# Performance work log

Hardware: AMD Instinct MI355X
Metric: run time of the kernel (lower is better)

Reference implementation:

```python
import jax, jax.numpy as jnp
import numpy as np

EMB = 1024
NH = 16
HD = EMB // NH
FF = 4 * EMB
B, T = 2, 2048
LN_EPS = 1e-5


def setup_inputs() -> dict:
    key = jax.random.key(0)
    ks = jax.random.split(key, 16)
    s = 0.02
    return {
        "x": jax.random.normal(ks[0], (B, T, EMB), jnp.float32),
        "wq": jax.random.normal(ks[1], (EMB, EMB), jnp.float32) * s,
        "bq": jnp.zeros((EMB,), jnp.float32),
        "wk": jax.random.normal(ks[2], (EMB, EMB), jnp.float32) * s,
        "bk": jnp.zeros((EMB,), jnp.float32),
        "wv": jax.random.normal(ks[3], (EMB, EMB), jnp.float32) * s,
        "bv": jnp.zeros((EMB,), jnp.float32),
        "wo": jax.random.normal(ks[4], (EMB, EMB), jnp.float32) * s,
        "bo": jnp.zeros((EMB,), jnp.float32),
        "w1": jax.random.normal(ks[5], (EMB, FF), jnp.float32) * s,
        "b1": jnp.zeros((FF,), jnp.float32),
        "w2": jax.random.normal(ks[6], (FF, EMB), jnp.float32) * s,
        "b2": jnp.zeros((EMB,), jnp.float32),
        "ln1_g": jnp.ones((EMB,), jnp.float32),
        "ln1_b": jnp.zeros((EMB,), jnp.float32),
        "ln2_g": jnp.ones((EMB,), jnp.float32),
        "ln2_b": jnp.zeros((EMB,), jnp.float32),
        "alpha_attn": jnp.float32(0.5),
        "alpha_ff": jnp.float32(0.5),
    }


def _layernorm(x, g, b):
    mu = jnp.mean(x, axis=-1, keepdims=True)
    var = jnp.var(x, axis=-1, keepdims=True)
    return (x - mu) * jax.lax.rsqrt(var + LN_EPS) * g + b


def reference(x, wq, bq, wk, bk, wv, bv, wo, bo, w1, b1, w2, b2,
              ln1_g, ln1_b, ln2_g, ln2_b, alpha_attn, alpha_ff):
    residual = x
    x_ = _layernorm(x, ln1_g, ln1_b)
    # [B,T,E] -> [B,H,T,D]
    def heads(y):
        return y.reshape(B, T, NH, HD).transpose(0, 2, 1, 3)
    q = heads(x_ @ wq + bq)
    k = heads(x_ @ wk + bk)
    v = heads(x_ @ wv + bv)
    scores = jnp.einsum("bhqd,bhkd->bhqk", q, k) / np.sqrt(HD).astype(np.float32)
    causal = jnp.tril(jnp.ones((T, T), dtype=bool))
    scores = jnp.where(causal, scores, -jnp.inf)
    attn = jax.nn.softmax(scores, axis=-1)  # dropout is identity in eval mode
    out = jnp.einsum("bhqk,bhkd->bhqd", attn, v)
    out = out.transpose(0, 2, 1, 3).reshape(B, T, EMB)
    out = out @ wo + bo
    x = residual + alpha_attn * out
    x2 = _layernorm(x, ln2_g, ln2_b)
    ff = jax.nn.gelu(x2 @ w1 + b1, approximate=False) @ w2 + b2
    return x + alpha_ff * ff
```

## Files before the change

### kernel.cpp

```cpp
#include <hip/hip_runtime.h>
#include <cmath>

#define EMB 1024
#define NH 16
#define HD 64
#define FF_DIM 4096
#define BB 2
#define TT 2048
#define NTOK (BB * TT)
#define QKVS 3072
#define SC2F 0.18033688011112042f

typedef _Float16 f16x8 __attribute__((ext_vector_type(8)));
typedef _Float16 f16x4 __attribute__((ext_vector_type(4)));
typedef float f32x4 __attribute__((ext_vector_type(4)));

__device__ __forceinline__ float gelu_fast(float x) {
    float u = x * (1.f + 0.044715f * x * x);
    float e = exp2f(u * 2.302118751f);
    return x - x / (e + 1.f);
}

template <typename TIN>
__global__ __launch_bounds__(256) void ln_kernel(const TIN* __restrict__ xin,
                                                 _Float16* __restrict__ out,
                                                 const float* __restrict__ g,
                                                 const float* __restrict__ bv) {
    int tid = threadIdx.x;
    size_t base = (size_t)blockIdx.x * EMB;
    float v[4];
#pragma unroll
    for (int i = 0; i < 4; ++i) v[i] = (float)xin[base + i * 256 + tid];
    float s = v[0] + v[1] + v[2] + v[3];
    float ss = v[0] * v[0] + v[1] * v[1] + v[2] * v[2] + v[3] * v[3];
#pragma unroll
    for (int off = 32; off > 0; off >>= 1) {
        s += __shfl_down(s, off);
        ss += __shfl_down(ss, off);
    }
    __shared__ float red[8];
    int wave = tid >> 6;
    if ((tid & 63) == 0) { red[wave] = s; red[4 + wave] = ss; }
    __syncthreads();
    s = red[0] + red[1] + red[2] + red[3];
    ss = red[4] + red[5] + red[6] + red[7];
    float mu = s * (1.0f / EMB);
    float var = ss * (1.0f / EMB) - mu * mu;
    float rstd = rsqrtf(var + 1e-5f);
#pragma unroll
    for (int i = 0; i < 4; ++i) {
        int idx = i * 256 + tid;
        float y = (v[i] - mu) * rstd * g[idx] + bv[idx];
        out[base + idx] = (_Float16)y;
    }
}

__global__ __launch_bounds__(256) void prep0_kernel(const float* __restrict__ x,
                                                    _Float16* __restrict__ xn,
                                                    const float* __restrict__ ln1_g,
                                                    const float* __restrict__ ln1_b,
                                                    const float* __restrict__ wq,
                                                    const float* __restrict__ wk,
                                                    const float* __restrict__ wv,
                                                    const float* __restrict__ wo,
                                                    const float* __restrict__ bq,
                                                    const float* __restrict__ bk,
                                                    const float* __restrict__ bv,
                                                    _Float16* __restrict__ wqkvT,
                                                    _Float16* __restrict__ woT,
                                                    float* __restrict__ qkvbias) {
    __shared__ float tile[32][33];
    int blk = blockIdx.x;
    int tid = threadIdx.x;
    if (blk >= 4108) {
        size_t base = (size_t)(blk - 4108) * EMB;
        float v[4];
#pragma unroll
        for (int i = 0; i < 4; ++i) v[i] = x[base + i * 256 + tid];
        float s = v[0] + v[1] + v[2] + v[3];
        float ss = v[0] * v[0] + v[1] * v[1] + v[2] * v[2] + v[3] * v[3];
#pragma unroll
        for (int off = 32; off > 0; off >>= 1) {
            s += __shfl_down(s, off);
            ss += __shfl_down(ss, off);
        }
        float* red = &tile[0][0];
        int wave = tid >> 6;
        if ((tid & 63) == 0) { red[wave] = s; red[4 + wave] = ss; }
        __syncthreads();
        s = red[0] + red[1] + red[2] + red[3];
        ss = red[4] + red[5] + red[6] + red[7];
        float mu = s * (1.0f / EMB);
        float var = ss * (1.0f / EMB) - mu * mu;
        float rstd = rsqrtf(var + 1e-5f);
#pragma unroll
        for (int i = 0; i < 4; ++i) {
            int idx = i * 256 + tid;
            xn[base + idx] = (_Float16)((v[i] - mu) * rstd * ln1_g[idx] + ln1_b[idx]);
        }
        return;
    }
    if (blk >= 4096) {
        int i = (blk - 4096) * 256 + tid;
        qkvbias[i] = i < 1024 ? bq[i] : (i < 2048 ? bk[i - 1024] : bv[i - 2048]);
        return;
    }
    const float* W;
    _Float16* Wt;
    int t = blk & 1023;
    int z = blk >> 10;
    if (z == 0) { W = wq; Wt = wqkvT; }
    else if (z == 1) { W = wk; Wt = wqkvT + 1024 * 1024; }
    else if (z == 2) { W = wv; Wt = wqkvT + 2 * 1024 * 1024; }
    else { W = wo; Wt = woT; }
    int bx = (t & 31) * 32, by = (t >> 5) * 32;
    int tx = tid & 31, ty = tid >> 5;
#pragma unroll
    for (int i = 0; i < 32; i += 8)
        tile[ty + i][tx] = W[(size_t)(by + ty + i) * EMB + bx + tx];
    __syncthreads();
#pragma unroll
    for (int i = 0; i < 32; i += 8)
        Wt[(size_t)(bx + ty + i) * EMB + by + tx] = (_Float16)tile[tx][ty + i];
}

__global__ __launch_bounds__(256) void prep2_kernel(const float* __restrict__ w1,
                                                    const float* __restrict__ w2,
                                                    _Float16* __restrict__ w1T,
                                                    _Float16* __restrict__ w2T) {
    int b = blockIdx.x;
    const float* W;
    _Float16* Wt;
    int K, N, t;
    if (b < 4096) { W = w1; Wt = w1T; K = 1024; N = 4096; t = b; }
    else { W = w2; Wt = w2T; K = 4096; N = 1024; t = b - 4096; }
    int ntx = N >> 5;
    int bx = (t % ntx) * 32, by = (t / ntx) * 32;
    __shared__ float tile[32][33];
    int tx = threadIdx.x & 31, ty = threadIdx.x >> 5;
#pragma unroll
    for (int i = 0; i < 32; i += 8)
        tile[ty + i][tx] = W[(size_t)(by + ty + i) * N + bx + tx];
    __syncthreads();
#pragma unroll
    for (int i = 0; i < 32; i += 8)
        Wt[(size_t)(bx + ty + i) * K + by + tx] = (_Float16)tile[tx][ty + i];
}

__global__ __launch_bounds__(256) void vT_kernel(const _Float16* __restrict__ qkv,
                                                 _Float16* __restrict__ VtG) {
    __shared__ _Float16 tile[64][72];
    int tid = threadIdx.x;
    int bh = blockIdx.y;
    int b = bh >> 4, h = bh & 15;
    int t0 = blockIdx.x * 64;
    const _Float16* src = qkv + (size_t)b * TT * QKVS + 2048 + h * HD;
    int r = tid >> 3;
    int c8 = (tid & 7) * 8;
#pragma unroll
    for (int p = 0; p < 2; ++p)
        *(f16x8*)(&tile[r + p * 32][c8]) =
            *(const f16x8*)(src + (size_t)(t0 + r + p * 32) * QKVS + c8);
    __syncthreads();
#pragma unroll
    for (int p = 0; p < 2; ++p) {
        int d = r + p * 32;
        f16x8 v;
#pragma unroll
        for (int j = 0; j < 8; ++j) v[j] = tile[c8 + j][d];
        *(f16x8*)(VtG + ((size_t)bh * HD + d) * TT + t0 + c8) = v;
    }
}

template <int MODE>
__global__ __launch_bounds__(256) void gemm_f16t(const _Float16* __restrict__ A,
                                                 const _Float16* __restrict__ Bt,
                                                 const float* __restrict__ bias,
                                                 void* __restrict__ outp,
                                                 void* __restrict__ vtg,
                                                 int M, int N, int K, int lda, int ldb) {
    __shared__ _Float16 As[128][64];
    __shared__ _Float16 Bs[128][64];
    int tid = threadIdx.x;
    int lane = tid & 63, w = tid >> 6;
    int quad = lane >> 4, l15 = lane & 15;
    int wm = (w >> 1) * 64, wn = (w & 1) * 64;
    int bM = blockIdx.y * 128, bN = blockIdx.x * 128;
    int lr = lane >> 3;
    int lcs = ((lane & 7) ^ lr) * 8;
    int sw = l15 & 7;
    f32x4 acc[4][4] = {};

    const _Float16* Abase = A + (size_t)(bM + w * 32 + lr) * lda + lcs;
    const _Float16* Bbase = Bt + (size_t)(bN + w * 32 + lr) * ldb + lcs;

    for (int kt = 0; kt < K; kt += 64) {
#pragma unroll
        for (int i = 0; i < 4; ++i) {
            __builtin_amdgcn_global_load_lds(
                (const __attribute__((address_space(1))) void*)(Abase + (size_t)(i * 8) * lda + kt),
                (__attribute__((address_space(3))) void*)(&As[w * 32 + i * 8][0]), 16, 0, 0);
            __builtin_amdgcn_global_load_lds(
                (const __attribute__((address_space(1))) void*)(Bbase + (size_t)(i * 8) * ldb + kt),
                (__attribute__((address_space(3))) void*)(&Bs[w * 32 + i * 8][0]), 16, 0, 0);
        }
        __syncthreads();
#pragma unroll
        for (int ks = 0; ks < 2; ++ks) {
            f16x8 af[4], bf[4];
#pragma unroll
            for (int i = 0; i < 4; ++i) {
                int sc = ((ks * 4 + quad) ^ sw) * 8;
                af[i] = *(const f16x8*)(&As[wm + i * 16 + l15][sc]);
                bf[i] = *(const f16x8*)(&Bs[wn + i * 16 + l15][sc]);
            }
#pragma unroll
            for (int i = 0; i < 4; ++i)
#pragma unroll
                for (int j = 0; j < 4; ++j)
                    acc[i][j] = __builtin_amdgcn_mfma_f32_16x16x32_f16(af[i], bf[j], acc[i][j], 0, 0, 0);
        }
        __syncthreads();
    }

    if (MODE == 6 && vtg != nullptr && bN >= 2048) {
        int bb = bM >> 11;
        int tbase = (bM & 2047) + wm;
#pragma unroll
        for (int i = 0; i < 4; ++i)
#pragma unroll
            for (int j = 0; j < 4; ++j) {
                int hd = bN - 2048 + wn + j * 16;
                int col = 2048 + hd + l15;
                _Float16* dst = (_Float16*)vtg +
                    (((size_t)(bb * 16 + (hd >> 6)) * 64) + (hd & 63) + l15) * TT +
                    tbase + i * 16 + quad * 4;
                f16x4 ov;
#pragma unroll
                for (int r = 0; r < 4; ++r) ov[r] = (_Float16)(acc[i][j][r] + bias[col]);
                *(f16x4*)dst = ov;
            }
        return;
    }

#pragma unroll
    for (int i = 0; i < 4; ++i)
#pragma unroll
        for (int j = 0; j < 4; ++j)
#pragma unroll
            for (int r = 0; r < 4; ++r) {
                int row = bM + wm + i * 16 + quad * 4 + r;
                int col = bN + wn + j * 16 + l15;
                size_t idx = (size_t)row * N + col;
                float vv = acc[i][j][r] + bias[col];
                if (MODE == 6) {
                    if (bN < 1024) vv *= SC2F;
                    ((_Float16*)outp)[idx] = (_Float16)vv;
                } else {
                    ((_Float16*)outp)[idx] = (_Float16)gelu_fast(vv);
                }
            }
}

#define STAGE_PAIR(OB, TN, I)                                                            \
    {                                                                                    \
        size_t ko = (size_t)(TN) * 64;                                                   \
        __builtin_amdgcn_global_load_lds(                                                \
            (const __attribute__((address_space(1))) void*)(Ab + (size_t)((I) * 8) * lda + ko), \
            (__attribute__((address_space(3))) void*)(&As[OB][w * 32 + (I) * 8][0]), 16, 0, 0); \
        __builtin_amdgcn_global_load_lds(                                                \
            (const __attribute__((address_space(1))) void*)(Bb + (size_t)((I) * 8) * ldb + ko), \
            (__attribute__((address_space(3))) void*)(&Bs[OB][w * 32 + (I) * 8][0]), 16, 0, 0); \
    }
#define RD_A(CB, I, KS) (*(const f16x8*)(&As[CB][wr * 128 + (I) * 16 + l15][(((KS)*4 + quad) ^ sw) * 8]))
#define RD_B(CB, J, KS) (*(const f16x8*)(&Bs[CB][wc * 64 + (J) * 16 + l15][(((KS)*4 + quad) ^ sw) * 8]))
#define MMQ(I0, J0)                                                                      \
    _Pragma("unroll") for (int ks = 0; ks < 2; ++ks) {                                   \
        _Pragma("unroll") for (int ii = 0; ii < 4; ++ii) {                               \
            _Pragma("unroll") for (int jj = 0; jj < 2; ++jj)                             \
                acc[(I0) + ii][(J0) + jj] = __builtin_amdgcn_mfma_f32_16x16x32_f16(      \
                    af[ii][ks], bf[(J0) + jj][ks], acc[(I0) + ii][(J0) + jj], 0, 0, 0);  \
        }                                                                                \
    }

template <int MODE>
__global__ __launch_bounds__(512, 2) void gemm256(const _Float16* __restrict__ A,
                                                  const _Float16* __restrict__ Bt,
                                                  const float* __restrict__ bias,
                                                  void* __restrict__ outp,
                                                  void* __restrict__ vtg,
                                                  int M, int N, int K, int lda, int ldb) {
    __shared__ _Float16 As[2][256][64];
    __shared__ _Float16 Bs[2][256][64];
    int tid = threadIdx.x;
    int lane = tid & 63, w = tid >> 6;
    int quad = lane >> 4, l15 = lane & 15;
    int wr = w >> 2, wc = w & 3;
    int gx = gridDim.x;
    int nwg = gx * gridDim.y;
    int bid = blockIdx.y * gx + blockIdx.x;
    int cpx = nwg >> 3;
    int sbid = (bid & 7) * cpx + (bid >> 3);
    int bN = (sbid % gx) * 256;
    int bM = (sbid / gx) * 256;
    int lr = lane >> 3;
    int lcs = ((lane & 7) ^ lr) * 8;
    int sw = l15 & 7;
    f32x4 acc[8][4] = {};
    f16x8 af[4][2], bf[4][2];

    const _Float16* Ab = A + (size_t)(bM + w * 32 + lr) * lda + lcs;
    const _Float16* Bb = Bt + (size_t)(bN + w * 32 + lr) * ldb + lcs;
    const int NT = K >> 6;

#pragma unroll
    for (int i = 0; i < 4; ++i) STAGE_PAIR(0, 0, i);
    asm volatile("s_waitcnt vmcnt(0)" ::: "memory");
    __builtin_amdgcn_s_barrier();

    int cur = 0;
    for (int t = 0; t < NT; ++t) {
        int nxt = cur ^ 1;
        int tn = (t + 1 < NT) ? t + 1 : 0;
#pragma unroll
        for (int i = 0; i < 4; ++i) STAGE_PAIR(nxt, tn, i);
#pragma unroll
        for (int i = 0; i < 4; ++i) {
            af[i][0] = RD_A(cur, i, 0);
            af[i][1] = RD_A(cur, i, 1);
        }
        bf[0][0] = RD_B(cur, 0, 0); bf[0][1] = RD_B(cur, 0, 1);
        bf[1][0] = RD_B(cur, 1, 0); bf[1][1] = RD_B(cur, 1, 1);
        MMQ(0, 0);
        bf[2][0] = RD_B(cur, 2, 0); bf[2][1] = RD_B(cur, 2, 1);
        bf[3][0] = RD_B(cur, 3, 0); bf[3][1] = RD_B(cur, 3, 1);
        MMQ(0, 2);
#pragma unroll
        for (int i = 0; i < 4; ++i) {
            af[i][0] = RD_A(cur, 4 + i, 0);
            af[i][1] = RD_A(cur, 4 + i, 1);
        }
        MMQ(4, 0);
        MMQ(4, 2);
        asm volatile("s_waitcnt vmcnt(0)" ::: "memory");
        __builtin_amdgcn_s_barrier();
        cur = nxt;
    }

    if (MODE == 1 && vtg != nullptr && bN >= 2048) {
        int bb = bM >> 11;
#pragma unroll
        for (int i = 0; i < 8; ++i)
#pragma unroll
            for (int j = 0; j < 4; ++j) {
                int hd = bN - 2048 + wc * 64 + j * 16;
                int col = 2048 + hd + l15;
                int tb = (bM & 2047) + wr * 128 + i * 16 + quad * 4;
                _Float16* dst = (_Float16*)vtg +
                    (((size_t)(bb * 16 + (hd >> 6)) * 64) + (hd & 63) + l15) * TT + tb;
                f16x4 ov;
#pragma unroll
                for (int r = 0; r < 4; ++r) ov[r] = (_Float16)(acc[i][j][r] + bias[col]);
                *(f16x4*)dst = ov;
            }
        return;
    }

#pragma unroll
    for (int i = 0; i < 8; ++i)
#pragma unroll
        for (int j = 0; j < 4; ++j)
#pragma unroll
            for (int r = 0; r < 4; ++r) {
                int row = bM + wr * 128 + i * 16 + quad * 4 + r;
                int col = bN + wc * 64 + j * 16 + l15;
                size_t idx = (size_t)row * N + col;
                float vv = acc[i][j][r] + bias[col];
                if (MODE == 1) {
                    if (bN < 1024) vv *= SC2F;
                    ((_Float16*)outp)[idx] = (_Float16)vv;
                } else {
                    ((_Float16*)outp)[idx] = (_Float16)gelu_fast(vv);
                }
            }
}

__global__ __launch_bounds__(512) void gemm_ff2(const _Float16* __restrict__ A,
                                                const _Float16* __restrict__ Bt,
                                                _Float16* __restrict__ p0,
                                                _Float16* __restrict__ p1,
                                                int M, int N, int K, int lda, int ldb) {
    __shared__ _Float16 As[2][256][64];
    __shared__ _Float16 Bs[2][128][64];
    int tid = threadIdx.x;
    int lane = tid & 63, w = tid >> 6;
    int quad = lane >> 4, l15 = lane & 15;
    int wr = w >> 1, wc = w & 1;
    int gx = gridDim.x;
    int nwg = gx * gridDim.y;
    int bid = blockIdx.y * gx + blockIdx.x;
    int cpx = nwg >> 3;
    int sbid = (bid & 7) * cpx + (bid >> 3);
    int bN = (sbid % gx) * 128;
    int bM = (sbid / gx) * 256;
    int kz = blockIdx.z * K;
    int lr = lane >> 3;
    int lcs = ((lane & 7) ^ lr) * 8;
    int sw = l15 & 7;
    f32x4 acc[4][4] = {};
    f16x8 af[4][2], bf[4][2];

    const _Float16* Ab = A + (size_t)(bM + w * 32 + lr) * lda + kz + lcs;
    const _Float16* Bb = Bt + (size_t)(bN + w * 16 + lr) * ldb + kz + lcs;
    const int NT = K >> 6;

#define FF2_STAGE(OB, TN)                                                                \
    {                                                                                    \
        size_t ko = (size_t)(TN) * 64;                                                   \
        _Pragma("unroll") for (int i = 0; i < 4; ++i)                                    \
            __builtin_amdgcn_global_load_lds(                                            \
                (const __attribute__((address_space(1))) void*)(Ab + (size_t)(i * 8) * lda + ko), \
                (__attribute__((address_space(3))) void*)(&As[OB][w * 32 + i * 8][0]), 16, 0, 0); \
        _Pragma("unroll") for (int i = 0; i < 2; ++i)                                    \
            __builtin_amdgcn_global_load_lds(                                            \
                (const __attribute__((address_space(1))) void*)(Bb + (size_t)(i * 8) * ldb + ko), \
                (__attribute__((address_space(3))) void*)(&Bs[OB][w * 16 + i * 8][0]), 16, 0, 0); \
    }

    FF2_STAGE(0, 0);
    asm volatile("s_waitcnt vmcnt(0)" ::: "memory");
    __builtin_amdgcn_s_barrier();

    int cur = 0;
    for (int t = 0; t < NT; ++t) {
        int nxt = cur ^ 1;
        int tn = (t + 1 < NT) ? t + 1 : 0;
        FF2_STAGE(nxt, tn);
#pragma unroll
        for (int i = 0; i < 4; ++i) {
#pragma unroll
            for (int ks = 0; ks < 2; ++ks)
                af[i][ks] = *(const f16x8*)(&As[cur][wr * 64 + i * 16 + l15][((ks * 4 + quad) ^ sw) * 8]);
        }
#pragma unroll
        for (int j = 0; j < 4; ++j) {
#pragma unroll
            for (int ks = 0; ks < 2; ++ks)
                bf[j][ks] = *(const f16x8*)(&Bs[cur][wc * 64 + j * 16 + l15][((ks * 4 + quad) ^ sw) * 8]);
        }
#pragma unroll
        for (int ks = 0; ks < 2; ++ks)
#pragma unroll
            for (int i = 0; i < 4; ++i)
#pragma unroll
                for (int j = 0; j < 4; ++j)
                    acc[i][j] = __builtin_amdgcn_mfma_f32_16x16x32_f16(af[i][ks], bf[j][ks], acc[i][j], 0, 0, 0);
        asm volatile("s_waitcnt vmcnt(0)" ::: "memory");
        __builtin_amdgcn_s_barrier();
        cur = nxt;
    }

    _Float16* pout = blockIdx.z ? p1 : p0;
#pragma unroll
    for (int i = 0; i < 4; ++i)
#pragma unroll
        for (int j = 0; j < 4; ++j)
#pragma unroll
            for (int r = 0; r < 4; ++r) {
                int row = bM + wr * 64 + i * 16 + quad * 4 + r;
                int col = bN + wc * 64 + j * 16 + l15;
                pout[(size_t)row * N + col] = (_Float16)acc[i][j][r];
            }
}

template <int MODE>
__global__ __launch_bounds__(256) void gemm64(const _Float16* __restrict__ A,
                                              const _Float16* __restrict__ Bt,
                                              const float* __restrict__ bias,
                                              void* __restrict__ outp,
                                              const void* __restrict__ residp,
                                              const float* __restrict__ alphap,
                                              int M, int N, int K, int lda, int ldb) {
    __shared__ _Float16 As[128][64];
    __shared__ _Float16 Bs[64][64];
    int tid = threadIdx.x;
    int lane = tid & 63, w = tid >> 6;
    int quad = lane >> 4, l15 = lane & 15;
    int wm = w * 32;
    int bM = blockIdx.y * 128, bN = blockIdx.x * 64;
    int lr = lane >> 3;
    int lcs = ((lane & 7) ^ lr) * 8;
    int sw = l15 & 7;
    f32x4 acc[2][4] = {};

    const _Float16* Abase = A + (size_t)(bM + w * 32 + lr) * lda + lcs;
    const _Float16* Bbase = Bt + (size_t)(bN + w * 16 + lr) * ldb + lcs;

    for (int kt = 0; kt < K; kt += 64) {
#pragma unroll
        for (int i = 0; i < 4; ++i)
            __builtin_amdgcn_global_load_lds(
                (const __attribute__((address_space(1))) void*)(Abase + (size_t)(i * 8) * lda + kt),
                (__attribute__((address_space(3))) void*)(&As[w * 32 + i * 8][0]), 16, 0, 0);
#pragma unroll
        for (int i = 0; i < 2; ++i)
            __builtin_amdgcn_global_load_lds(
                (const __attribute__((address_space(1))) void*)(Bbase + (size_t)(i * 8) * ldb + kt),
                (__attribute__((address_space(3))) void*)(&Bs[w * 16 + i * 8][0]), 16, 0, 0);
        __syncthreads();
#pragma unroll
        for (int ks = 0; ks < 2; ++ks) {
            int sc = ((ks * 4 + quad) ^ sw) * 8;
            f16x8 af[2], bf[4];
#pragma unroll
            for (int i = 0; i < 2; ++i)
                af[i] = *(const f16x8*)(&As[wm + i * 16 + l15][sc]);
#pragma unroll
            for (int j = 0; j < 4; ++j)
                bf[j] = *(const f16x8*)(&Bs[j * 16 + l15][sc]);
#pragma unroll
            for (int i = 0; i < 2; ++i)
#pragma unroll
                for (int j = 0; j < 4; ++j)
                    acc[i][j] = __builtin_amdgcn_mfma_f32_16x16x32_f16(af[i], bf[j], acc[i][j], 0, 0, 0);
        }
        __syncthreads();
    }

    float alpha = 0.f;
    if (MODE == 2 || MODE == 5) alpha = alphap[0];
#pragma unroll
    for (int i = 0; i < 2; ++i)
#pragma unroll
        for (int j = 0; j < 4; ++j)
#pragma unroll
            for (int r = 0; r < 4; ++r) {
                int row = bM + wm + i * 16 + quad * 4 + r;
                int col = bN + j * 16 + l15;
                size_t idx = (size_t)row * N + col;
                if (MODE == 4) {
                    ((float*)outp)[idx] = acc[i][j][r];
                } else if (MODE == 2) {
                    float vv = acc[i][j][r] + bias[col];
                    float rsd = ((const float*)residp)[idx];
                    ((_Float16*)outp)[idx] = (_Float16)(rsd + alpha * vv);
                } else {
                    float vv = acc[i][j][r] + bias[col];
                    float prev = ((float*)outp)[idx];
                    float rsd = (float)((const _Float16*)residp)[idx];
                    ((float*)outp)[idx] = rsd + alpha * (prev + vv);
                }
            }
}

__global__ __launch_bounds__(256) void ff2_reduce_kernel(const _Float16* __restrict__ p0,
                                                         const _Float16* __restrict__ p1,
                                                         const _Float16* __restrict__ xmid,
                                                         const float* __restrict__ b2,
                                                         const float* __restrict__ alphap,
                                                         float* __restrict__ out) {
    int i = (blockIdx.x * 256 + threadIdx.x) * 8;
    float alpha = alphap[0];
    f16x8 a = *(const f16x8*)(p0 + i);
    f16x8 b = *(const f16x8*)(p1 + i);
    f16x8 xm = *(const f16x8*)(xmid + i);
    int col = i & 1023;
#pragma unroll
    for (int k = 0; k < 8; ++k)
        out[i + k] = (float)xm[k] + alpha * ((float)a[k] + (float)b[k] + b2[col + k]);
}

#define QT 64
#define NEG_BIG (-1e30f)
__global__ __launch_bounds__(512) void attn_mfma_kernel(const _Float16* __restrict__ qkv,
                                                        const _Float16* __restrict__ VtG,
                                                        _Float16* __restrict__ O) {
    __shared__ _Float16 Ks[64][72];
    __shared__ _Float16 Vt[64][72];
    __shared__ _Float16 Ps[8][16][68];
    int tid = threadIdx.x;
    int lane = tid & 63, w = tid >> 6;
    int quad = lane >> 4, l15 = lane & 15;
    int bh = blockIdx.x;
    int b = bh >> 4, h = bh & 15;
    int y = blockIdx.y;
    int seg = w >> 2, ws = w & 3;
    int qt = seg ? y : (31 - y);
    int q0 = qt * QT;
    int ntw = qt + 1;
    int ntmax = 32 - y;
    const _Float16* Qh = qkv + (size_t)b * TT * QKVS + h * HD;
    const _Float16* Kh = Qh + 1024;
    const _Float16* Vrows = VtG + (size_t)bh * HD * TT;

    int m0 = q0 + ws * 16;
    f16x8 aq0 = *(const f16x8*)(Qh + (size_t)(m0 + l15) * QKVS + quad * 8);
    f16x8 aq1 = *(const f16x8*)(Qh + (size_t)(m0 + l15) * QKVS + 32 + quad * 8);

    f32x4 Oacc[4] = {};
    float lrow[4] = {0.f, 0.f, 0.f, 0.f};

    int rr = tid >> 3;
    int c8 = (tid & 7) * 8;
    const _Float16* Kp = Kh + (size_t)rr * QKVS + c8;
    const _Float16* Vp = Vrows + (size_t)rr * TT + c8;

    f16x8 kreg = *(const f16x8*)(Kp);
    f16x8 vreg = *(const f16x8*)(Vp);

    for (int t = 0; t < ntmax; ++t) {
        int t0 = t * 64;
        __syncthreads();
        *(f16x8*)(&Ks[rr][c8]) = kreg;
        *(f16x8*)(&Vt[rr][c8]) = vreg;
        __syncthreads();
        if (t + 1 < ntmax) {
            kreg = *(const f16x8*)(Kp + (size_t)(t0 + 64) * QKVS);
            vreg = *(const f16x8*)(Vp + t0 + 64);
        }
        if (t >= ntw) continue;

        f32x4 Sacc[4] = {};
        __builtin_amdgcn_s_setprio(1);
#pragma unroll
        for (int nc = 0; nc < 4; ++nc) {
            f16x8 bk0 = *(const f16x8*)(&Ks[nc * 16 + l15][quad * 8]);
            f16x8 bk1 = *(const f16x8*)(&Ks[nc * 16 + l15][32 + quad * 8]);
            Sacc[nc] = __builtin_amdgcn_mfma_f32_16x16x32_f16(aq0, bk0, Sacc[nc], 0, 0, 0);
            Sacc[nc] = __builtin_amdgcn_mfma_f32_16x16x32_f16(aq1, bk1, Sacc[nc], 0, 0, 0);
        }
        __builtin_amdgcn_s_setprio(0);

        if (t0 == q0) {
#pragma unroll
            for (int nc = 0; nc < 4; ++nc) {
                int key = t0 + nc * 16 + l15;
#pragma unroll
                for (int i = 0; i < 4; ++i)
                    if (key > m0 + quad * 4 + i) Sacc[nc][i] = NEG_BIG;
            }
        }

#pragma unroll
        for (int nc = 0; nc < 4; ++nc)
#pragma unroll
            for (int i = 0; i < 4; ++i) {
                float p = exp2f(Sacc[nc][i]);
                lrow[i] += p;
                Ps[w][quad * 4 + i][nc * 16 + l15] = (_Float16)p;
            }
        __asm__ __volatile__("s_waitcnt lgkmcnt(0)" ::: "memory");

        f16x8 ap0 = *(const f16x8*)(&Ps[w][l15][quad * 8]);
        f16x8 ap1 = *(const f16x8*)(&Ps[w][l15][32 + quad * 8]);
        __builtin_amdgcn_s_setprio(1);
#pragma unroll
        for (int nc = 0; nc < 4; ++nc) {
            int d = nc * 16 + l15;
            f16x8 bv0 = *(const f16x8*)(&Vt[d][quad * 8]);
            f16x8 bv1 = *(const f16x8*)(&Vt[d][32 + quad * 8]);
            Oacc[nc] = __builtin_amdgcn_mfma_f32_16x16x32_f16(ap0, bv0, Oacc[nc], 0, 0, 0);
            Oacc[nc] = __builtin_amdgcn_mfma_f32_16x16x32_f16(ap1, bv1, Oacc[nc], 0, 0, 0);
        }
        __builtin_amdgcn_s_setprio(0);
    }

#pragma unroll
    for (int off = 1; off < 16; off <<= 1)
#pragma unroll
        for (int i = 0; i < 4; ++i) lrow[i] += __shfl_xor(lrow[i], off);
#pragma unroll
    for (int i = 0; i < 4; ++i) lrow[i] = 1.0f / lrow[i];
    _Float16* Oh = O + (size_t)b * TT * EMB + h * HD;
#pragma unroll
    for (int nc = 0; nc < 4; ++nc)
#pragma unroll
        for (int i = 0; i < 4; ++i) {
            int row = m0 + quad * 4 + i;
            Oh[(size_t)row * EMB + nc * 16 + l15] = (_Float16)(Oacc[nc][i] * lrow[i]);
        }
}

extern "C" void kernel_launch(void* const* d_in, const int* in_sizes, int n_in,
                              void* d_out, int out_size, void* d_ws, size_t ws_size,
                              hipStream_t stream) {
    const float* x = (const float*)d_in[0];
    const float* wq = (const float*)d_in[1];
    const float* bq = (const float*)d_in[2];
    const float* wk = (const float*)d_in[3];
    const float* bk = (const float*)d_in[4];
    const float* wv = (const float*)d_in[5];
    const float* bv = (const float*)d_in[6];
    const float* wo = (const float*)d_in[7];
    const float* bo = (const float*)d_in[8];
    const float* w1 = (const float*)d_in[9];
    const float* b1 = (const float*)d_in[10];
    const float* w2 = (const float*)d_in[11];
    const float* b2 = (const float*)d_in[12];
    const float* ln1_g = (const float*)d_in[13];
    const float* ln1_b = (const float*)d_in[14];
    const float* ln2_g = (const float*)d_in[15];
    const float* ln2_b = (const float*)d_in[16];
    const float* alpha_attn = (const float*)d_in[17];
    const float* alpha_ff = (const float*)d_in[18];

    const size_t SL = (size_t)8 * 1024 * 1024;
    char* ws = (char*)d_ws;
    _Float16* xn = (_Float16*)(ws);
    _Float16* qkv = (_Float16*)(ws + SL);
    _Float16* wqkvT = (_Float16*)(ws + 4 * SL);
    float* qkvbias = (float*)(ws + 4 * SL + 6 * 1024 * 1024);
    _Float16* attnout = (_Float16*)(ws);
    _Float16* xmid = (_Float16*)(ws + SL);
    _Float16* x2 = (_Float16*)(ws + 2 * SL);
    _Float16* w1T = (_Float16*)(ws);
    _Float16* w2T = (_Float16*)(ws + 3 * SL);
    _Float16* ff1 = (_Float16*)(ws + 4 * SL);
    bool bigws = ws_size >= (size_t)64 * 1024 * 1024;
    _Float16* VtG = bigws ? (_Float16*)(ws + 5 * SL) : (_Float16*)(ws + 4 * SL);
    _Float16* woT = bigws ? (_Float16*)(ws + 6 * SL) : (_Float16*)(ws + 5 * SL);
    _Float16* part0 = (_Float16*)(ws);
    _Float16* part1 = (_Float16*)(ws + 2 * SL);

    prep0_kernel<<<8204, 256, 0, stream>>>(x, xn, ln1_g, ln1_b, wq, wk, wv, wo,
                                           bq, bk, bv, wqkvT, woT, qkvbias);

    if (bigws) {
        gemm256<1><<<dim3(QKVS / 256, NTOK / 256), 512, 0, stream>>>(
            xn, wqkvT, qkvbias, qkv, (void*)VtG, NTOK, QKVS, EMB, EMB, EMB);
    } else {
        gemm_f16t<6><<<dim3(QKVS / 128, NTOK / 128), 256, 0, stream>>>(
            xn, wqkvT, qkvbias, qkv, nullptr, NTOK, QKVS, EMB, EMB, EMB);
        vT_kernel<<<dim3(TT / 64, BB * NH), 256, 0, stream>>>(qkv, VtG);
    }

    attn_mfma_kernel<<<dim3(BB * NH, TT / QT / 2), 512, 0, stream>>>(qkv, VtG, attnout);

    gemm64<2><<<dim3(EMB / 64, NTOK / 128), 256, 0, stream>>>(
        attnout, woT, bo, xmid, x, alpha_attn, NTOK, EMB, EMB, EMB, EMB);

    ln_kernel<_Float16><<<NTOK, 256, 0, stream>>>(xmid, x2, ln2_g, ln2_b);

    prep2_kernel<<<8192, 256, 0, stream>>>(w1, w2, w1T, w2T);

    if (bigws) {
        gemm256<0><<<dim3(FF_DIM / 256, NTOK / 256), 512, 0, stream>>>(
            x2, w1T, b1, ff1, nullptr, NTOK, FF_DIM, EMB, EMB, EMB);
        gemm_ff2<<<dim3(EMB / 128, NTOK / 256, 2), 512, 0, stream>>>(
            ff1, w2T, part0, part1, NTOK, EMB, 2048, FF_DIM, FF_DIM);
        ff2_reduce_kernel<<<NTOK * EMB / 8 / 256, 256, 0, stream>>>(
            part0, part1, xmid, b2, alpha_ff, (float*)d_out);
    } else {
        const int NC = 2048;
        for (int hh = 0; hh < 2; ++hh) {
            const _Float16* w1Th = w1T + (size_t)hh * NC * EMB;
            const _Float16* w2Th = w2T + (size_t)hh * NC;
            gemm_f16t<1><<<dim3(NC / 128, NTOK / 128), 256, 0, stream>>>(
                x2, w1Th, b1 + hh * NC, ff1, nullptr, NTOK, NC, EMB, EMB, EMB);
            if (hh == 0)
                gemm64<4><<<dim3(EMB / 64, NTOK / 128), 256, 0, stream>>>(
                    ff1, w2Th, nullptr, d_out, nullptr, nullptr, NTOK, EMB, NC, NC, FF_DIM);
            else
                gemm64<5><<<dim3(EMB / 64, NTOK / 128), 256, 0, stream>>>(
                    ff1, w2Th, b2, d_out, xmid, alpha_ff, NTOK, EMB, NC, NC, FF_DIM);
        }
    }
}
```

Before: 343.9 us.

## Retile FF2 split-K GEMM to 128x128 blocks with XCD-aware block mapping

The second feed-forward GEMM (split-K by two) now uses 128x128 tiles with 256 threads instead of 256x128 tiles with 512 threads. It runs as a flat grid of 512 blocks, where each block's XCD index selects the K half and an M quarter. The aim is to double the number of blocks for better CU occupancy and to keep blocks that share operands on the same XCD for L2 reuse. In exchange, per-block operand reuse drops, and the dimensions (2048 split, 32 K-tiles) are hard-coded.

```diff
diff --git a/kernel.cpp b/kernel.cpp
--- a/kernel.cpp
+++ b/kernel.cpp
@@ -385,25 +385,26 @@
             }
 }
 
-__global__ __launch_bounds__(512) void gemm_ff2(const _Float16* __restrict__ A,
+__global__ __launch_bounds__(256) void gemm_ff2(const _Float16* __restrict__ A,
                                                 const _Float16* __restrict__ Bt,
                                                 _Float16* __restrict__ p0,
                                                 _Float16* __restrict__ p1,
                                                 int M, int N, int K, int lda, int ldb) {
-    __shared__ _Float16 As[2][256][64];
+    __shared__ _Float16 As[2][128][64];
     __shared__ _Float16 Bs[2][128][64];
     int tid = threadIdx.x;
     int lane = tid & 63, w = tid >> 6;
     int quad = lane >> 4, l15 = lane & 15;
-    int wr = w >> 1, wc = w & 1;
-    int gx = gridDim.x;
-    int nwg = gx * gridDim.y;
-    int bid = blockIdx.y * gx + blockIdx.x;
-    int cpx = nwg >> 3;
-    int sbid = (bid & 7) * cpx + (bid >> 3);
-    int bN = (sbid % gx) * 128;
-    int bM = (sbid / gx) * 256;
-    int kz = blockIdx.z * K;
+    int wr = (w >> 1) * 64, wc = (w & 1) * 64;
+    int bid = blockIdx.x;
+    int xcd = bid & 7;
+    int j = bid >> 3;
+    int zz = xcd >> 2;
+    int mq = xcd & 3;
+    int n = j & 7;
+    int m = (j >> 3) + mq * 8;
+    int bM = m * 128, bN = n * 128;
+    int kz = zz * 2048;
     int lr = lane >> 3;
     int lcs = ((lane & 7) ^ lr) * 8;
     int sw = l15 & 7;
@@ -411,20 +412,20 @@
     f16x8 af[4][2], bf[4][2];
 
     const _Float16* Ab = A + (size_t)(bM + w * 32 + lr) * lda + kz + lcs;
-    const _Float16* Bb = Bt + (size_t)(bN + w * 16 + lr) * ldb + kz + lcs;
-    const int NT = K >> 6;
+    const _Float16* Bb = Bt + (size_t)(bN + w * 32 + lr) * ldb + kz + lcs;
+    const int NT = 32;
 
 #define FF2_STAGE(OB, TN)                                                                \
     {                                                                                    \
         size_t ko = (size_t)(TN) * 64;                                                   \
-        _Pragma("unroll") for (int i = 0; i < 4; ++i)                                    \
+        _Pragma("unroll") for (int i = 0; i < 4; ++i) {                                  \
             __builtin_amdgcn_global_load_lds(                                            \
                 (const __attribute__((address_space(1))) void*)(Ab + (size_t)(i * 8) * lda + ko), \
                 (__attribute__((address_space(3))) void*)(&As[OB][w * 32 + i * 8][0]), 16, 0, 0); \
-        _Pragma("unroll") for (int i = 0; i < 2; ++i)                                    \
             __builtin_amdgcn_global_load_lds(                                            \
                 (const __attribute__((address_space(1))) void*)(Bb + (size_t)(i * 8) * ldb + ko), \
-                (__attribute__((address_space(3))) void*)(&Bs[OB][w * 16 + i * 8][0]), 16, 0, 0); \
+                (__attribute__((address_space(3))) void*)(&Bs[OB][w * 32 + i * 8][0]), 16, 0, 0); \
+        }                                                                                \
     }
 
     FF2_STAGE(0, 0);
@@ -440,36 +441,36 @@
         for (int i = 0; i < 4; ++i) {
 #pragma unroll
             for (int ks = 0; ks < 2; ++ks)
-                af[i][ks] = *(const f16x8*)(&As[cur][wr * 64 + i * 16 + l15][((ks * 4 + quad) ^ sw) * 8]);
-        }
-#pragma unroll
-        for (int j = 0; j < 4; ++j) {
+                af[i][ks] = *(const f16x8*)(&As[cur][wr + i * 16 + l15][((ks * 4 + quad) ^ sw) * 8]);
+        }
+#pragma unroll
+        for (int jj = 0; jj < 4; ++jj) {
 #pragma unroll
             for (int ks = 0; ks < 2; ++ks)
-                bf[j][ks] = *(const f16x8*)(&Bs[cur][wc * 64 + j * 16 + l15][((ks * 4 + quad) ^ sw) * 8]);
+                bf[jj][ks] = *(const f16x8*)(&Bs[cur][wc + jj * 16 + l15][((ks * 4 + quad) ^ sw) * 8]);
         }
 #pragma unroll
         for (int ks = 0; ks < 2; ++ks)
 #pragma unroll
             for (int i = 0; i < 4; ++i)
 #pragma unroll
-                for (int j = 0; j < 4; ++j)
-                    acc[i][j] = __builtin_amdgcn_mfma_f32_16x16x32_f16(af[i][ks], bf[j][ks], acc[i][j], 0, 0, 0);
+                for (int jj = 0; jj < 4; ++jj)
+                    acc[i][jj] = __builtin_amdgcn_mfma_f32_16x16x32_f16(af[i][ks], bf[jj][ks], acc[i][jj], 0, 0, 0);
         asm volatile("s_waitcnt vmcnt(0)" ::: "memory");
         __builtin_amdgcn_s_barrier();
         cur = nxt;
     }
 
-    _Float16* pout = blockIdx.z ? p1 : p0;
+    _Float16* pout = zz ? p1 : p0;
 #pragma unroll
     for (int i = 0; i < 4; ++i)
 #pragma unroll
-        for (int j = 0; j < 4; ++j)
+        for (int jj = 0; jj < 4; ++jj)
 #pragma unroll
             for (int r = 0; r < 4; ++r) {
-                int row = bM + wr * 64 + i * 16 + quad * 4 + r;
-                int col = bN + wc * 64 + j * 16 + l15;
-                pout[(size_t)row * N + col] = (_Float16)acc[i][j][r];
+                int row = bM + wr + i * 16 + quad * 4 + r;
+                int col = bN + wc + jj * 16 + l15;
+                pout[(size_t)row * N + col] = (_Float16)acc[i][jj][r];
             }
 }
 
@@ -746,8 +747,8 @@
     if (bigws) {
         gemm256<0><<<dim3(FF_DIM / 256, NTOK / 256), 512, 0, stream>>>(
             x2, w1T, b1, ff1, nullptr, NTOK, FF_DIM, EMB, EMB, EMB);
-        gemm_ff2<<<dim3(EMB / 128, NTOK / 256, 2), 512, 0, stream>>>(
-            ff1, w2T, part0, part1, NTOK, EMB, 2048, FF_DIM, FF_DIM);
+        gemm_ff2<<<512, 256, 0, stream>>>(
+            ff1, w2T, part0, part1, NTOK, EMB, FF_DIM, FF_DIM, FF_DIM);
         ff2_reduce_kernel<<<NTOK * EMB / 8 / 256, 256, 0, stream>>>(
             part0, part1, xmid, b2, alpha_ff, (float*)d_out);
     } else {
```

After: 326.9 us. 1.05x faster.
